# Optimization experiments

Hardware: AMD Instinct MI355X
Metric: run time of the kernel (lower is better)

## Reference

```python
import jax, jax.numpy as jnp
import numpy as np

R, D, H, NLAYERS = 128, 64, 64, 3
B, N = 64, 1024
INIT_W = 0.1


def setup_inputs() -> dict:
    key = jax.random.key(0)
    ks = jax.random.split(key, 10)
    x = jax.random.normal(ks[0], (B, D, N), dtype=jnp.float32)
    L = jax.random.randint(ks[1], (B, 1, N), 0, 2, dtype=jnp.int32)
    wq0 = INIT_W * jax.random.normal(ks[2], (R, D), dtype=jnp.float32)
    wqr = INIT_W * jax.random.normal(ks[3], (NLAYERS - 1, R, R), dtype=jnp.float32)
    wk0 = INIT_W * jax.random.normal(ks[4], (R, D), dtype=jnp.float32)
    wkr = INIT_W * jax.random.normal(ks[5], (NLAYERS - 1, R, R), dtype=jnp.float32)
    wv0 = INIT_W * jax.random.normal(ks[6], (R, D), dtype=jnp.float32)
    wvr = INIT_W * jax.random.normal(ks[7], (NLAYERS - 1, R, R), dtype=jnp.float32)
    wor = INIT_W * jax.random.normal(ks[8], (NLAYERS - 1, R, R), dtype=jnp.float32)
    wo_last = INIT_W * jax.random.normal(ks[9], (H, R), dtype=jnp.float32)
    return {"x": x, "L": L, "wq0": wq0, "wqr": wqr, "wk0": wk0, "wkr": wkr,
            "wv0": wv0, "wvr": wvr, "wor": wor, "wo_last": wo_last}


def reference(x, L, wq0, wqr, wk0, wkr, wv0, wvr, wor, wo_last):
    # x: [B, d, N]; L: [B, 1, N] neighbor mask (first row used)
    Lrow = L[:, 0, :].astype(jnp.float32)                      # [B, N]
    num_neighbors = jnp.sum((Lrow >= 1).astype(jnp.float32), axis=1)[:, None, None] + 1.0  # [B,1,1]
    scale = jnp.sqrt(num_neighbors)
    mask = Lrow[:, None, :]                                    # [B, 1, N], broadcast over r

    inp = x
    for layer in range(NLAYERS):
        Wq = wq0 if layer == 0 else wqr[layer - 1]
        Wk = wk0 if layer == 0 else wkr[layer - 1]
        Wv = wv0 if layer == 0 else wvr[layer - 1]
        # sigmoid-gated projections: [B, r, N]
        Q = jax.nn.sigmoid(jnp.einsum('rd,bdn->brn', Wq, inp))
        K = jax.nn.sigmoid(jnp.einsum('rd,bdn->brn', Wk, inp))
        V = jax.nn.sigmoid(jnp.einsum('rd,bdn->brn', Wv, inp))
        # degree-scaled softmax attention over agents: scores [B, N, N]
        A = jax.nn.softmax(jnp.einsum('brn,brm->bnm', Q, K) / scale, axis=-1)
        # o[b,r,n] = sum_m A[b,n,m] * V[b,r,m]  -> [B, r, N]
        o = jnp.einsum('bnm,brm->brn', A, V)
        Wo = wor[layer] if layer < NLAYERS - 1 else wo_last
        inp = jax.nn.silu(jnp.einsum('or,brn->bon', Wo, o))
        if layer != NLAYERS - 1:  # remask_bias=True
            inp = mask * inp
    return inp  # [B, h, N]
```

## Files before the change

kernel.cpp:

```cpp
#include <hip/hip_runtime.h>


typedef __bf16 bf16;
typedef bf16 bf16x2 __attribute__((ext_vector_type(2)));
typedef bf16 bf16x4 __attribute__((ext_vector_type(4)));
typedef bf16 bf16x8 __attribute__((ext_vector_type(8)));
typedef float f32x4 __attribute__((ext_vector_type(4)));
typedef float f32x16 __attribute__((ext_vector_type(16)));
typedef unsigned int u32;
typedef u32 u32x4 __attribute__((ext_vector_type(4)));

#define MFMA32(a, b, c) __builtin_amdgcn_mfma_f32_32x32x16_bf16(a, b, c, 0, 0, 0)
#define ZERO16 {0,0,0,0,0,0,0,0,0,0,0,0,0,0,0,0}
#define LOG2E 1.44269504f

__device__ __forceinline__ float fast_exp2(float x) {
  return __builtin_amdgcn_exp2f(x);
}
__device__ __forceinline__ float fast_sigmoid(float x) {
  return __builtin_amdgcn_rcpf(1.0f + fast_exp2(-LOG2E * x));
}
__device__ __forceinline__ u32 cvt_pk_bf16(float lo, float hi) {
  u32 r;
  asm("v_cvt_pk_bf16_f32 %0, %1, %2" : "=v"(r) : "v"(lo), "v"(hi));
  return r;
}
__device__ __forceinline__ void pl32_swap(u32& a, u32& b) {
  asm("v_permlane32_swap_b32 %0, %1" : "+v"(a), "+v"(b));
}
__device__ __forceinline__ void build_frags(const f32x16 v, bf16x8& f0, bf16x8& f1) {
  u32 t0 = cvt_pk_bf16(v[0], v[1]);
  u32 t1 = cvt_pk_bf16(v[2], v[3]);
  u32 t2 = cvt_pk_bf16(v[4], v[5]);
  u32 t3 = cvt_pk_bf16(v[6], v[7]);
  pl32_swap(t0, t2);
  pl32_swap(t1, t3);
  u32x4 a = {t0, t1, t2, t3};
  f0 = __builtin_bit_cast(bf16x8, a);
  u32 s0 = cvt_pk_bf16(v[8], v[9]);
  u32 s1 = cvt_pk_bf16(v[10], v[11]);
  u32 s2 = cvt_pk_bf16(v[12], v[13]);
  u32 s3 = cvt_pk_bf16(v[14], v[15]);
  pl32_swap(s0, s2);
  pl32_swap(s1, s3);
  u32x4 c = {s0, s1, s2, s3};
  f1 = __builtin_bit_cast(bf16x8, c);
}

__global__ __launch_bounds__(256) void prep_kernel(
    const int* __restrict__ L,
    const float* __restrict__ wq0, const float* __restrict__ wqr,
    const float* __restrict__ wk0, const float* __restrict__ wkr,
    const float* __restrict__ wv0, const float* __restrict__ wvr,
    const float* __restrict__ wor, const float* __restrict__ wo_last,
    float* __restrict__ scale_inv, float* __restrict__ biasv,
    bf16* __restrict__ wbf) {
  __shared__ int red[256];
  const int blk = blockIdx.x;
  const int tid = threadIdx.x;
  if (blk < 64) {
    int cnt = 0;
    for (int n = tid; n < 1024; n += 256) cnt += (L[blk * 1024 + n] >= 1) ? 1 : 0;
    red[tid] = cnt;
    __syncthreads();
    for (int s = 128; s > 0; s >>= 1) {
      if (tid < s) red[tid] += red[tid + s];
      __syncthreads();
    }
    if (tid == 0) {
      float iv = rsqrtf((float)red[0] + 1.0f);
      scale_inv[blk] = iv;
      biasv[blk] = fmaxf(0.0f, 128.0f * iv * LOG2E - 80.0f);
    }
  } else {
    for (int i = (blk - 64) * 256 + tid; i < 163840; i += 64 * 256) {
      float v;
      if      (i <   8192) v = wq0[i];
      else if (i <  40960) v = wqr[i - 8192];
      else if (i <  49152) v = wk0[i - 40960];
      else if (i <  81920) v = wkr[i - 49152];
      else if (i <  90112) v = wv0[i - 81920];
      else if (i < 122880) v = wvr[i - 90112];
      else if (i < 155648) v = wor[i - 122880];
      else                 v = wo_last[i - 155648];
      wbf[i] = (bf16)v;
    }
  }
}

__global__ __launch_bounds__(256) void xk0_kernel(
    const float* __restrict__ x, const bf16* __restrict__ Wk,
    const bf16* __restrict__ Wv, bf16* __restrict__ xT,
    bf16* __restrict__ Kt, bf16* __restrict__ Vn) {
  __shared__ float tile[64][65];
  __shared__ __attribute__((aligned(16))) bf16 inp_lds[64 * 72];
  const int tid = threadIdx.x;
  const int lane = tid & 63, wv = tid >> 6;
  const int la = lane & 31, hi = lane >> 5;
  const int b = blockIdx.x >> 4;
  const int t0 = (blockIdx.x & 15) * 64;

  {
    const int nl = tid & 63, dbase = (tid >> 6) * 16;
#pragma unroll
    for (int i = 0; i < 16; i++) {
      int d = dbase + i;
      tile[d][nl] = x[(size_t)(b * 64 + d) * 1024 + t0 + nl];
    }
  }
  __syncthreads();
  {
    const int dl = (tid & 31) * 2, nb = (tid >> 5) * 8;
#pragma unroll
    for (int i = 0; i < 8; i++) {
      int n = nb + i;
      bf16x2 pr = {(bf16)tile[dl][n], (bf16)tile[dl + 1][n]};
      *(bf16x2*)(xT + (size_t)(b * 1024 + t0 + n) * 64 + dl) = pr;
      *(bf16x2*)&inp_lds[n * 72 + dl] = pr;
    }
  }
  __syncthreads();

  const int sub = wv & 1;
  if (wv < 2) {
#pragma unroll
    for (int rt2 = 0; rt2 < 2; rt2++) {
      const int rt = 2 * sub + rt2;
      bf16x8 wf[4];
#pragma unroll
      for (int ks = 0; ks < 4; ks++)
        wf[ks] = *(const bf16x8*)(Wk + (size_t)(la + 32 * rt) * 64 + hi * 8 + ks * 16);
#pragma unroll
      for (int tt = 0; tt < 2; tt++) {
        f32x16 acc = ZERO16;
#pragma unroll
        for (int ks = 0; ks < 4; ks++) {
          bf16x8 bfr = *(const bf16x8*)&inp_lds[(la + 32 * tt) * 72 + hi * 8 + ks * 16];
          acc = MFMA32(wf[ks], bfr, acc);
        }
#pragma unroll
        for (int g = 0; g < 4; g++) {
          bf16x4 pk;
#pragma unroll
          for (int i = 0; i < 4; i++) pk[i] = (bf16)fast_sigmoid(acc[4 * g + i]);
          *(bf16x4*)(Kt + (size_t)(b * 1024 + t0 + 32 * tt + la) * 128 +
                     32 * rt + 8 * g + 4 * hi) = pk;
        }
      }
    }
  } else {
#pragma unroll
    for (int rc2 = 0; rc2 < 2; rc2++) {
      const int rc = 2 * sub + rc2;
      bf16x8 wf[4];
#pragma unroll
      for (int ks = 0; ks < 4; ks++)
        wf[ks] = *(const bf16x8*)(Wv + (size_t)(la + 32 * rc) * 64 + hi * 8 + ks * 16);
#pragma unroll
      for (int tt = 0; tt < 2; tt++) {
        f32x16 acc = ZERO16;
#pragma unroll
        for (int ks = 0; ks < 4; ks++) {
          bf16x8 afr = *(const bf16x8*)&inp_lds[(la + 32 * tt) * 72 + hi * 8 + ks * 16];
          acc = MFMA32(afr, wf[ks], acc);
        }
#pragma unroll
        for (int g = 0; g < 4; g++) {
          bf16x4 pk;
#pragma unroll
          for (int i = 0; i < 4; i++) pk[i] = (bf16)fast_sigmoid(acc[4 * g + i]);
          *(bf16x4*)(Vn + (size_t)(b * 128 + la + 32 * rc) * 1024 +
                     t0 + 32 * tt + 8 * g + 4 * hi) = pk;
        }
      }
    }
  }
}

template <int DIN>
__global__ __launch_bounds__(256) void kv_kernel(
    const bf16* __restrict__ inpT, const bf16* __restrict__ Wk,
    const bf16* __restrict__ Wv, bf16* __restrict__ Kt,
    bf16* __restrict__ Vn) {
  constexpr int SIN = DIN + 8;
  constexpr int KS = DIN / 16;
  constexpr int CPR = DIN / 8;
  __shared__ __attribute__((aligned(16))) bf16 inp_lds[64 * SIN];
  const int tid = threadIdx.x;
  const int lane = tid & 63, wv = tid >> 6;
  const int la = lane & 31, hi = lane >> 5;
  const int b = blockIdx.x >> 4;
  const int t0 = (blockIdx.x & 15) * 64;

  for (int i = tid; i < 64 * CPR; i += 256) {
    int row = i / CPR, c = i % CPR;
    *(bf16x8*)&inp_lds[row * SIN + c * 8] =
        *(const bf16x8*)(inpT + (size_t)(b * 1024 + t0 + row) * DIN + c * 8);
  }
  __syncthreads();

  const int sub = wv & 1;
  if (wv < 2) {
#pragma unroll
    for (int rt2 = 0; rt2 < 2; rt2++) {
      const int rt = 2 * sub + rt2;
      bf16x8 wf[KS];
#pragma unroll
      for (int ks = 0; ks < KS; ks++)
        wf[ks] = *(const bf16x8*)(Wk + (size_t)(la + 32 * rt) * DIN + hi * 8 + ks * 16);
#pragma unroll
      for (int tt = 0; tt < 2; tt++) {
        f32x16 acc = ZERO16;
#pragma unroll
        for (int ks = 0; ks < KS; ks++) {
          bf16x8 bfr = *(const bf16x8*)&inp_lds[(la + 32 * tt) * SIN + hi * 8 + ks * 16];
          acc = MFMA32(wf[ks], bfr, acc);
        }
#pragma unroll
        for (int g = 0; g < 4; g++) {
          bf16x4 pk;
#pragma unroll
          for (int i = 0; i < 4; i++) pk[i] = (bf16)fast_sigmoid(acc[4 * g + i]);
          *(bf16x4*)(Kt + (size_t)(b * 1024 + t0 + 32 * tt + la) * 128 +
                     32 * rt + 8 * g + 4 * hi) = pk;
        }
      }
    }
  } else {
#pragma unroll
    for (int rc2 = 0; rc2 < 2; rc2++) {
      const int rc = 2 * sub + rc2;
      bf16x8 wf[KS];
#pragma unroll
      for (int ks = 0; ks < KS; ks++)
        wf[ks] = *(const bf16x8*)(Wv + (size_t)(la + 32 * rc) * DIN + hi * 8 + ks * 16);
#pragma unroll
      for (int tt = 0; tt < 2; tt++) {
        f32x16 acc = ZERO16;
#pragma unroll
        for (int ks = 0; ks < KS; ks++) {
          bf16x8 afr = *(const bf16x8*)&inp_lds[(la + 32 * tt) * SIN + hi * 8 + ks * 16];
          acc = MFMA32(afr, wf[ks], acc);
        }
#pragma unroll
        for (int g = 0; g < 4; g++) {
          bf16x4 pk;
#pragma unroll
          for (int i = 0; i < 4; i++) pk[i] = (bf16)fast_sigmoid(acc[4 * g + i]);
          *(bf16x4*)(Vn + (size_t)(b * 128 + 32 * rc + la) * 1024 +
                     t0 + 32 * tt + 8 * g + 4 * hi) = pk;
        }
      }
    }
  }
}

template <int DIN>
__global__ __launch_bounds__(256, 2) void flash_kernel(
    const bf16* __restrict__ inpT, const bf16* __restrict__ Wq,
    const bf16* __restrict__ Kt, const bf16* __restrict__ Vn,
    const float* __restrict__ scale_inv, const float* __restrict__ biasv,
    const int* __restrict__ L, const bf16* __restrict__ Wo,
    void* __restrict__ outp, int last,
    const bf16* __restrict__ Wkn, const bf16* __restrict__ Wvn,
    bf16* __restrict__ Ktn, bf16* __restrict__ Vnn, int kvgen) {
  __shared__ __attribute__((aligned(16))) char smem[71680];

  const int tid = threadIdx.x;
  const int lane = tid & 63, wv = tid >> 6;
  const int la = lane & 31, hi = lane >> 5;
  const int xcd = blockIdx.x & 7;
  const int kk = blockIdx.x >> 3;
  const int b = xcd * 8 + (kk & 7);
  const int q0 = (kk >> 3) * 128;

  const float inv2 = scale_inv[b] * LOG2E;
  const float bb = biasv[b];

  const int krow = tid >> 4, kc = (tid & 15) * 8;
  const int vrow = tid >> 3, vc = (tid & 7) * 8;
  const bf16* kbase = Kt + (size_t)b * 1024 * 128;
  const bf16* vbase = Vn + (size_t)b * 128 * 1024;

  bf16x8 kr[4], vr[4];
#pragma unroll
  for (int p = 0; p < 4; p++) {
    kr[p] = *(const bf16x8*)(kbase + (size_t)(krow + 16 * p) * 128 + kc);
    vr[p] = *(const bf16x8*)(vbase + (size_t)(vrow + 32 * p) * 1024 + vc);
  }

  bf16x8 qB[8];
  {
    constexpr int SIN = DIN + 8;
    constexpr int KSD = DIN / 16;
    constexpr int CPR = DIN / 8;
    bf16* inp_s = (bf16*)smem;
    for (int i = tid; i < 128 * CPR; i += 256) {
      int row = i / CPR, c = i % CPR;
      *(bf16x8*)&inp_s[row * SIN + c * 8] =
          *(const bf16x8*)(inpT + (size_t)(b * 1024 + q0 + row) * DIN + c * 8);
    }
    __syncthreads();
    bf16x8 bfr[KSD];
#pragma unroll
    for (int ks = 0; ks < KSD; ks++)
      bfr[ks] = *(const bf16x8*)&inp_s[(32 * wv + la) * SIN + hi * 8 + ks * 16];
#pragma unroll
    for (int rt = 0; rt < 4; rt++) {
      f32x16 acc = ZERO16;
#pragma unroll
      for (int ks = 0; ks < KSD; ks++) {
        bf16x8 wf = *(const bf16x8*)(Wq + (size_t)(32 * rt + la) * DIN +
                                     hi * 8 + ks * 16);
        acc = MFMA32(wf, bfr[ks], acc);
      }
      f32x16 qv;
#pragma unroll
      for (int j = 0; j < 16; j++) qv[j] = fast_sigmoid(acc[j]) * inv2;
      build_frags(qv, qB[2 * rt], qB[2 * rt + 1]);
    }
    __syncthreads();
  }

  {
    bf16* K0 = (bf16*)smem;
    bf16* V0 = (bf16*)(smem + 34816);
#pragma unroll
    for (int p = 0; p < 4; p++) *(bf16x8*)&K0[(krow + 16 * p) * 136 + kc] = kr[p];
#pragma unroll
    for (int p = 0; p < 4; p++) *(bf16x8*)&V0[(vrow + 32 * p) * 72 + vc] = vr[p];
#pragma unroll
    for (int p = 0; p < 4; p++) {
      kr[p] = *(const bf16x8*)(kbase + (size_t)(64 + krow + 16 * p) * 128 + kc);
      vr[p] = *(const bf16x8*)(vbase + (size_t)(vrow + 32 * p) * 1024 + 64 + vc);
    }
    __syncthreads();
  }

  f32x16 acc_o[4] = {ZERO16, ZERO16, ZERO16, ZERO16};
  float rs = 0.f;

  for (int it = 0; it < 16; it++) {
    const int cur = it & 1;
    const bf16* Kc = (const bf16*)(smem + cur * 17408);
    const bf16* Vc = (const bf16*)(smem + 34816 + cur * 18432);
    if (it < 15) {
      bf16* Kn = (bf16*)(smem + (1 - cur) * 17408);
      bf16* Vx = (bf16*)(smem + 34816 + (1 - cur) * 18432);
#pragma unroll
      for (int p = 0; p < 4; p++)
        *(bf16x8*)&Kn[(krow + 16 * p) * 136 + kc] = kr[p];
#pragma unroll
      for (int p = 0; p < 4; p++)
        *(bf16x8*)&Vx[(vrow + 32 * p) * 72 + vc] = vr[p];
    }
    if (it < 14) {
      const int m2 = (it + 2) * 64;
#pragma unroll
      for (int p = 0; p < 4; p++) {
        kr[p] = *(const bf16x8*)(kbase + (size_t)(m2 + krow + 16 * p) * 128 + kc);
        vr[p] = *(const bf16x8*)(vbase + (size_t)(vrow + 32 * p) * 1024 + m2 + vc);
      }
    }

    bf16x8 pa[4];
#pragma unroll
    for (int kt = 0; kt < 2; kt++) {
      f32x16 sa = ZERO16;
#pragma unroll
      for (int ks = 0; ks < 8; ks++) {
        bf16x8 kf = *(const bf16x8*)&Kc[(32 * kt + la) * 136 + hi * 8 + ks * 16];
        sa = MFMA32(kf, qB[ks], sa);
      }
      f32x16 pv;
#pragma unroll
      for (int j = 0; j < 16; j++) {
        float p = fast_exp2(sa[j] - bb);
        rs += p;
        pv[j] = p;
      }
      build_frags(pv, pa[2 * kt], pa[2 * kt + 1]);
    }

#pragma unroll
    for (int rt = 0; rt < 4; rt++) {
#pragma unroll
      for (int k2 = 0; k2 < 4; k2++) {
        bf16x8 vB = *(const bf16x8*)&Vc[(32 * rt + la) * 72 + hi * 8 + k2 * 16];
        acc_o[rt] = MFMA32(pa[k2], vB, acc_o[rt]);
      }
    }
    __syncthreads();
  }

  rs += __shfl_xor(rs, 32, 64);
  float* rsp = (float*)(smem + 34816);
  if (lane < 32) rsp[32 * wv + la] = rs;
  bf16* O_lds = (bf16*)smem;
#pragma unroll
  for (int g = 0; g < 4; g++) {
    const int qb = 8 * g + 4 * hi;
    f32x4 r4 = *(f32x4*)&rsp[32 * wv + qb];
    f32x4 is;
#pragma unroll
    for (int i = 0; i < 4; i++) is[i] = 1.0f / r4[i];
#pragma unroll
    for (int rt = 0; rt < 4; rt++) {
#pragma unroll
      for (int i = 0; i < 4; i++) {
        O_lds[(size_t)(32 * wv + qb + i) * 136 + 32 * rt + la] =
            (bf16)(acc_o[rt][4 * g + i] * is[i]);
      }
    }
  }
  __syncthreads();

  if (!last) {
    bf16* out_b = (bf16*)outp;
    bf16* O2 = (bf16*)(smem + 36864);
    const int* Lg = L + b * 1024 + q0;
    bf16x8 wB[8];
#pragma unroll
    for (int ks = 0; ks < 8; ks++)
      wB[ks] = *(const bf16x8*)(Wo + (size_t)(la + 32 * wv) * 128 + hi * 8 + ks * 16);
#pragma unroll
    for (int nt = 0; nt < 4; nt++) {
      f32x16 acc = ZERO16;
#pragma unroll
      for (int ks = 0; ks < 8; ks++) {
        bf16x8 oA = *(const bf16x8*)&O_lds[(size_t)(la + 32 * nt) * 136 +
                                           hi * 8 + ks * 16];
        acc = MFMA32(oA, wB[ks], acc);
      }
#pragma unroll
      for (int g = 0; g < 4; g++) {
#pragma unroll
        for (int i = 0; i < 4; i++) {
          int n = 32 * nt + 8 * g + 4 * hi + i;
          float xv = acc[4 * g + i];
          float y = xv * fast_sigmoid(xv) * (float)Lg[n];
          out_b[(size_t)(b * 1024 + q0 + n) * 128 + 32 * wv + la] = (bf16)y;
          if (kvgen) O2[(size_t)n * 136 + 32 * wv + la] = (bf16)y;
        }
      }
    }
    if (kvgen) {
      __syncthreads();
      const bf16* O2c = (const bf16*)(smem + 36864);
      const int sub = wv & 1;
      const bf16* W2 = (wv < 2) ? Wkn : Wvn;
#pragma unroll
      for (int rt2 = 0; rt2 < 2; rt2++) {
        const int rt = 2 * sub + rt2;
        bf16x8 wf[8];
#pragma unroll
        for (int ks = 0; ks < 8; ks++)
          wf[ks] = *(const bf16x8*)(W2 + (size_t)(la + 32 * rt) * 128 +
                                    hi * 8 + ks * 16);
#pragma unroll
        for (int tt = 0; tt < 4; tt++) {
          f32x16 acc = ZERO16;
          if (wv < 2) {
#pragma unroll
            for (int ks = 0; ks < 8; ks++) {
              bf16x8 bB = *(const bf16x8*)&O2c[(size_t)(32 * tt + la) * 136 +
                                               hi * 8 + ks * 16];
              acc = MFMA32(wf[ks], bB, acc);
            }
#pragma unroll
            for (int g = 0; g < 4; g++) {
              bf16x4 pk;
#pragma unroll
              for (int i = 0; i < 4; i++) pk[i] = (bf16)fast_sigmoid(acc[4 * g + i]);
              *(bf16x4*)(Ktn + (size_t)(b * 1024 + q0 + 32 * tt + la) * 128 +
                         32 * rt + 8 * g + 4 * hi) = pk;
            }
          } else {
#pragma unroll
            for (int ks = 0; ks < 8; ks++) {
              bf16x8 aA = *(const bf16x8*)&O2c[(size_t)(32 * tt + la) * 136 +
                                               hi * 8 + ks * 16];
              acc = MFMA32(aA, wf[ks], acc);
            }
#pragma unroll
            for (int g = 0; g < 4; g++) {
              bf16x4 pk;
#pragma unroll
              for (int i = 0; i < 4; i++) pk[i] = (bf16)fast_sigmoid(acc[4 * g + i]);
              *(bf16x4*)(Vnn + (size_t)(b * 128 + 32 * rt + la) * 1024 +
                         q0 + 32 * tt + 8 * g + 4 * hi) = pk;
            }
          }
        }
      }
    }
  } else {
    const int hs = wv & 1, nq = wv >> 1;
    float* outf = (float*)outp;
    bf16x8 wA[8];
#pragma unroll
    for (int ks = 0; ks < 8; ks++)
      wA[ks] = *(const bf16x8*)(Wo + (size_t)(la + 32 * hs) * 128 + hi * 8 + ks * 16);
#pragma unroll
    for (int t = 0; t < 2; t++) {
      const int ns4 = nq + 2 * t;
      f32x16 acc = ZERO16;
#pragma unroll
      for (int ks = 0; ks < 8; ks++) {
        bf16x8 oB = *(const bf16x8*)&O_lds[(size_t)(32 * ns4 + la) * 136 +
                                           hi * 8 + ks * 16];
        acc = MFMA32(wA[ks], oB, acc);
      }
#pragma unroll
      for (int g = 0; g < 4; g++) {
#pragma unroll
        for (int i = 0; i < 4; i++) {
          int h = 32 * hs + 8 * g + 4 * hi + i;
          float xv = acc[4 * g + i];
          outf[(size_t)(b * 64 + h) * 1024 + q0 + 32 * ns4 + la] =
              xv * fast_sigmoid(xv);
        }
      }
    }
  }
}

__global__ __launch_bounds__(256) void xpose_kernel(const float* __restrict__ x,
                                                    bf16* __restrict__ xT) {
  __shared__ float tile[64][65];
  const int blk = blockIdx.x;
  const int b = blk >> 4;
  const int n0 = (blk & 15) * 64;
  const int tid = threadIdx.x;
  {
    const int nl = tid & 63, dbase = (tid >> 6) * 16;
#pragma unroll
    for (int i = 0; i < 16; i++) {
      int d = dbase + i;
      tile[d][nl] = x[(size_t)(b * 64 + d) * 1024 + n0 + nl];
    }
  }
  __syncthreads();
  {
    const int dl = (tid & 31) * 2, nb = (tid >> 5) * 8;
#pragma unroll
    for (int i = 0; i < 8; i++) {
      int n = nb + i;
      bf16x2 pr = {(bf16)tile[dl][n], (bf16)tile[dl + 1][n]};
      *(bf16x2*)(xT + (size_t)(b * 1024 + n0 + n) * 64 + dl) = pr;
    }
  }
}

extern "C" void kernel_launch(void* const* d_in, const int* in_sizes, int n_in,
                              void* d_out, int out_size, void* d_ws, size_t ws_size,
                              hipStream_t stream) {
  const float* x = (const float*)d_in[0];
  const int* L = (const int*)d_in[1];
  const float* wq0 = (const float*)d_in[2];
  const float* wqr = (const float*)d_in[3];
  const float* wk0 = (const float*)d_in[4];
  const float* wkr = (const float*)d_in[5];
  const float* wv0 = (const float*)d_in[6];
  const float* wvr = (const float*)d_in[7];
  const float* wor = (const float*)d_in[8];
  const float* wo_last = (const float*)d_in[9];

  char* ws = (char*)d_ws;
  float* scale_inv = (float*)(ws + 0);
  float* biasv = (float*)(ws + 1024);
  bf16* wbf = (bf16*)(ws + 4096);
  bf16* xT = (bf16*)(ws + 335872);
  bf16* inpT = (bf16*)(ws + 8724480);
  bf16* KtA = (bf16*)(ws + 25501696);
  bf16* VnA = (bf16*)(ws + 42278912);
  bf16* KtB = (bf16*)(ws + 59056128);
  bf16* VnB = (bf16*)(ws + 75833344);

  prep_kernel<<<128, 256, 0, stream>>>(L, wq0, wqr, wk0, wkr, wv0, wvr, wor,
                                       wo_last, scale_inv, biasv, wbf);

  if (ws_size >= 92610560) {
    xk0_kernel<<<1024, 256, 0, stream>>>(x, wbf + 40960, wbf + 81920, xT, KtA, VnA);
    flash_kernel<64><<<512, 256, 0, stream>>>(
        xT, wbf + 0, KtA, VnA, scale_inv, biasv, L, wbf + 122880, (void*)inpT, 0,
        wbf + 49152, wbf + 90112, KtB, VnB, 1);
    flash_kernel<128><<<512, 256, 0, stream>>>(
        inpT, wbf + 8192, KtB, VnB, scale_inv, biasv, L, wbf + 139264,
        (void*)inpT, 0, wbf + 65536, wbf + 106496, KtA, VnA, 1);
    flash_kernel<128><<<512, 256, 0, stream>>>(
        inpT, wbf + 24576, KtA, VnA, scale_inv, biasv, L, wbf + 155648, d_out, 1,
        nullptr, nullptr, nullptr, nullptr, 0);
  } else if (ws_size >= 59056128) {
    xpose_kernel<<<1024, 256, 0, stream>>>(x, xT);
    for (int l = 0; l < 3; l++) {
      const bf16* Wq = (l == 0) ? wbf + 0 : wbf + 8192 + (size_t)(l - 1) * 16384;
      const bf16* Wk = (l == 0) ? wbf + 40960 : wbf + 49152 + (size_t)(l - 1) * 16384;
      const bf16* Wv = (l == 0) ? wbf + 81920 : wbf + 90112 + (size_t)(l - 1) * 16384;
      const bf16* Wo = (l < 2) ? wbf + 122880 + (size_t)l * 16384 : wbf + 155648;
      void* outp = (l < 2) ? (void*)inpT : (void*)d_out;
      if (l == 0) {
        kv_kernel<64><<<1024, 256, 0, stream>>>(xT, Wk, Wv, KtA, VnA);
        flash_kernel<64><<<512, 256, 0, stream>>>(xT, Wq, KtA, VnA, scale_inv,
                                                  biasv, L, Wo, outp, 0,
                                                  nullptr, nullptr, nullptr,
                                                  nullptr, 0);
      } else {
        kv_kernel<128><<<1024, 256, 0, stream>>>(inpT, Wk, Wv, KtA, VnA);
        flash_kernel<128><<<512, 256, 0, stream>>>(inpT, Wq, KtA, VnA, scale_inv,
                                                   biasv, L, Wo, outp,
                                                   (l == 2) ? 1 : 0, nullptr,
                                                   nullptr, nullptr, nullptr, 0);
      }
    }
  }
}
```

Measured before the change: 273.6 us.

## Split flash kernel into 64-query tiles with intra-block KV split and reduction

Each block now handles 64 queries instead of 128, and the grid doubles to 1024 blocks. Inside a block, the four waves split into two query tiles and two key halves, and the key-half partial outputs and row sums are combined through LDS at the end. The K/V double buffer is replaced by a single buffer with two barriers per step, halving shared memory so launch bounds can request three blocks per CU. The aim is more parallelism and occupancy, at the cost of extra synchronisation, a cross-wave reduction, and twice the K/V global reads per query.

```diff
diff --git a/kernel.cpp b/kernel.cpp
--- a/kernel.cpp
+++ b/kernel.cpp
@@ -45,6 +45,12 @@
   pl32_swap(s1, s3);
   u32x4 c = {s0, s1, s2, s3};
   f1 = __builtin_bit_cast(bf16x8, c);
+}
+__device__ __forceinline__ float treesum16(const f32x16 v) {
+  float a0 = v[0] + v[1], a1 = v[2] + v[3], a2 = v[4] + v[5], a3 = v[6] + v[7];
+  float a4 = v[8] + v[9], a5 = v[10] + v[11], a6 = v[12] + v[13], a7 = v[14] + v[15];
+  float b0 = a0 + a1, b1 = a2 + a3, b2 = a4 + a5, b3 = a6 + a7;
+  return (b0 + b1) + (b2 + b3);
 }
 
 __global__ __launch_bounds__(256) void prep_kernel(
@@ -256,7 +262,7 @@
 }
 
 template <int DIN>
-__global__ __launch_bounds__(256, 2) void flash_kernel(
+__global__ __launch_bounds__(256, 3) void flash_kernel(
     const bf16* __restrict__ inpT, const bf16* __restrict__ Wq,
     const bf16* __restrict__ Kt, const bf16* __restrict__ Vn,
     const float* __restrict__ scale_inv, const float* __restrict__ biasv,
@@ -264,15 +270,16 @@
     void* __restrict__ outp, int last,
     const bf16* __restrict__ Wkn, const bf16* __restrict__ Wvn,
     bf16* __restrict__ Ktn, bf16* __restrict__ Vnn, int kvgen) {
-  __shared__ __attribute__((aligned(16))) char smem[71680];
+  __shared__ __attribute__((aligned(16))) char smem[35840];
 
   const int tid = threadIdx.x;
   const int lane = tid & 63, wv = tid >> 6;
   const int la = lane & 31, hi = lane >> 5;
+  const int qt = wv & 1, kg = wv >> 1;
   const int xcd = blockIdx.x & 7;
   const int kk = blockIdx.x >> 3;
   const int b = xcd * 8 + (kk & 7);
-  const int q0 = (kk >> 3) * 128;
+  const int q0 = (kk >> 3) * 64;
 
   const float inv2 = scale_inv[b] * LOG2E;
   const float bb = biasv[b];
@@ -295,7 +302,7 @@
     constexpr int KSD = DIN / 16;
     constexpr int CPR = DIN / 8;
     bf16* inp_s = (bf16*)smem;
-    for (int i = tid; i < 128 * CPR; i += 256) {
+    for (int i = tid; i < 64 * CPR; i += 256) {
       int row = i / CPR, c = i % CPR;
       *(bf16x8*)&inp_s[row * SIN + c * 8] =
           *(const bf16x8*)(inpT + (size_t)(b * 1024 + q0 + row) * DIN + c * 8);
@@ -304,7 +311,7 @@
     bf16x8 bfr[KSD];
 #pragma unroll
     for (int ks = 0; ks < KSD; ks++)
-      bfr[ks] = *(const bf16x8*)&inp_s[(32 * wv + la) * SIN + hi * 8 + ks * 16];
+      bfr[ks] = *(const bf16x8*)&inp_s[(32 * qt + la) * SIN + hi * 8 + ks * 16];
 #pragma unroll
     for (int rt = 0; rt < 4; rt++) {
       f32x16 acc = ZERO16;
@@ -319,97 +326,107 @@
       for (int j = 0; j < 16; j++) qv[j] = fast_sigmoid(acc[j]) * inv2;
       build_frags(qv, qB[2 * rt], qB[2 * rt + 1]);
     }
-    __syncthreads();
-  }
-
-  {
-    bf16* K0 = (bf16*)smem;
-    bf16* V0 = (bf16*)(smem + 34816);
-#pragma unroll
-    for (int p = 0; p < 4; p++) *(bf16x8*)&K0[(krow + 16 * p) * 136 + kc] = kr[p];
-#pragma unroll
-    for (int p = 0; p < 4; p++) *(bf16x8*)&V0[(vrow + 32 * p) * 72 + vc] = vr[p];
-#pragma unroll
-    for (int p = 0; p < 4; p++) {
-      kr[p] = *(const bf16x8*)(kbase + (size_t)(64 + krow + 16 * p) * 128 + kc);
-      vr[p] = *(const bf16x8*)(vbase + (size_t)(vrow + 32 * p) * 1024 + 64 + vc);
-    }
-    __syncthreads();
-  }
-
+  }
+
+  bf16* K_lds = (bf16*)smem;
+  bf16* V_lds = (bf16*)(smem + 17408);
   f32x16 acc_o[4] = {ZERO16, ZERO16, ZERO16, ZERO16};
   float rs = 0.f;
 
   for (int it = 0; it < 16; it++) {
-    const int cur = it & 1;
-    const bf16* Kc = (const bf16*)(smem + cur * 17408);
-    const bf16* Vc = (const bf16*)(smem + 34816 + cur * 18432);
+    __syncthreads();
+#pragma unroll
+    for (int p = 0; p < 4; p++)
+      *(bf16x8*)&K_lds[(krow + 16 * p) * 136 + kc] = kr[p];
+#pragma unroll
+    for (int p = 0; p < 4; p++)
+      *(bf16x8*)&V_lds[(vrow + 32 * p) * 72 + vc] = vr[p];
+    __syncthreads();
+
+    f32x16 sa = ZERO16;
+#pragma unroll
+    for (int ks = 0; ks < 8; ks++) {
+      bf16x8 kf = *(const bf16x8*)&K_lds[(32 * kg + la) * 136 + hi * 8 + ks * 16];
+      sa = MFMA32(kf, qB[ks], sa);
+    }
+
+    f32x16 pv;
+#pragma unroll
+    for (int j = 0; j < 16; j++) pv[j] = fast_exp2(sa[j] - bb);
+    rs += treesum16(pv);
+    bf16x8 pa[2];
+    build_frags(pv, pa[0], pa[1]);
+
     if (it < 15) {
-      bf16* Kn = (bf16*)(smem + (1 - cur) * 17408);
-      bf16* Vx = (bf16*)(smem + 34816 + (1 - cur) * 18432);
-#pragma unroll
-      for (int p = 0; p < 4; p++)
-        *(bf16x8*)&Kn[(krow + 16 * p) * 136 + kc] = kr[p];
-#pragma unroll
-      for (int p = 0; p < 4; p++)
-        *(bf16x8*)&Vx[(vrow + 32 * p) * 72 + vc] = vr[p];
-    }
-    if (it < 14) {
-      const int m2 = (it + 2) * 64;
+      const int m1 = (it + 1) * 64;
 #pragma unroll
       for (int p = 0; p < 4; p++) {
-        kr[p] = *(const bf16x8*)(kbase + (size_t)(m2 + krow + 16 * p) * 128 + kc);
-        vr[p] = *(const bf16x8*)(vbase + (size_t)(vrow + 32 * p) * 1024 + m2 + vc);
-      }
-    }
-
-    bf16x8 pa[4];
-#pragma unroll
-    for (int kt = 0; kt < 2; kt++) {
-      f32x16 sa = ZERO16;
-#pragma unroll
-      for (int ks = 0; ks < 8; ks++) {
-        bf16x8 kf = *(const bf16x8*)&Kc[(32 * kt + la) * 136 + hi * 8 + ks * 16];
-        sa = MFMA32(kf, qB[ks], sa);
-      }
-      f32x16 pv;
-#pragma unroll
-      for (int j = 0; j < 16; j++) {
-        float p = fast_exp2(sa[j] - bb);
-        rs += p;
-        pv[j] = p;
-      }
-      build_frags(pv, pa[2 * kt], pa[2 * kt + 1]);
+        kr[p] = *(const bf16x8*)(kbase + (size_t)(m1 + krow + 16 * p) * 128 + kc);
+        vr[p] = *(const bf16x8*)(vbase + (size_t)(vrow + 32 * p) * 1024 + m1 + vc);
+      }
     }
 
 #pragma unroll
     for (int rt = 0; rt < 4; rt++) {
 #pragma unroll
-      for (int k2 = 0; k2 < 4; k2++) {
-        bf16x8 vB = *(const bf16x8*)&Vc[(32 * rt + la) * 72 + hi * 8 + k2 * 16];
+      for (int k2 = 0; k2 < 2; k2++) {
+        bf16x8 vB = *(const bf16x8*)&V_lds[(32 * rt + la) * 72 +
+                                           32 * kg + 16 * k2 + 8 * hi];
         acc_o[rt] = MFMA32(pa[k2], vB, acc_o[rt]);
       }
     }
-    __syncthreads();
   }
 
   rs += __shfl_xor(rs, 32, 64);
-  float* rsp = (float*)(smem + 34816);
-  if (lane < 32) rsp[32 * wv + la] = rs;
+  float* hand = (float*)smem;
+  float* rsc = (float*)(smem + 34816);
+  __syncthreads();
+  if (kg) {
+    float* dst = hand + qt * 4352 + lane * 68;
+#pragma unroll
+    for (int rt = 0; rt < 4; rt++) {
+#pragma unroll
+      for (int q4 = 0; q4 < 4; q4++) {
+        f32x4 t = {acc_o[rt][4 * q4], acc_o[rt][4 * q4 + 1],
+                   acc_o[rt][4 * q4 + 2], acc_o[rt][4 * q4 + 3]};
+        *(f32x4*)(dst + 16 * rt + 4 * q4) = t;
+      }
+    }
+    if (lane < 32) rsc[qt * 32 + la] = rs;
+  }
+  __syncthreads();
+  if (kg == 0) {
+    const float* src = hand + qt * 4352 + lane * 68;
+#pragma unroll
+    for (int rt = 0; rt < 4; rt++) {
+#pragma unroll
+      for (int q4 = 0; q4 < 4; q4++) {
+        f32x4 t = *(const f32x4*)(src + 16 * rt + 4 * q4);
+#pragma unroll
+        for (int i = 0; i < 4; i++) acc_o[rt][4 * q4 + i] += t[i];
+      }
+    }
+    rs += rsc[qt * 32 + la];
+    if (lane < 32) rsc[qt * 32 + la] = rs;
+  }
+  __syncthreads();
+
   bf16* O_lds = (bf16*)smem;
-#pragma unroll
-  for (int g = 0; g < 4; g++) {
-    const int qb = 8 * g + 4 * hi;
-    f32x4 r4 = *(f32x4*)&rsp[32 * wv + qb];
-    f32x4 is;
-#pragma unroll
-    for (int i = 0; i < 4; i++) is[i] = 1.0f / r4[i];
-#pragma unroll
-    for (int rt = 0; rt < 4; rt++) {
-#pragma unroll
-      for (int i = 0; i < 4; i++) {
-        O_lds[(size_t)(32 * wv + qb + i) * 136 + 32 * rt + la] =
-            (bf16)(acc_o[rt][4 * g + i] * is[i]);
+  if (kg == 0) {
+#pragma unroll
+    for (int g = 0; g < 4; g++) {
+      const int qb = 8 * g + 4 * hi;
+      f32x4 r4 = *(f32x4*)&rsc[32 * qt + qb];
+      f32x4 is;
+#pragma unroll
+      for (int i = 0; i < 4; i++) is[i] = 1.0f / r4[i];
+#pragma unroll
+      for (int rt = 0; rt < 4; rt++) {
+#pragma unroll
+        for (int i = 0; i < 4; i++) {
+          O_lds[(size_t)(32 * qt + qb + i) * 136 + 32 * rt + la] =
+              (bf16)(acc_o[rt][4 * g + i] * is[i]);
+        }
       }
     }
   }
@@ -417,18 +434,18 @@
 
   if (!last) {
     bf16* out_b = (bf16*)outp;
-    bf16* O2 = (bf16*)(smem + 36864);
+    bf16* O2 = (bf16*)(smem + 17408);
     const int* Lg = L + b * 1024 + q0;
     bf16x8 wB[8];
 #pragma unroll
     for (int ks = 0; ks < 8; ks++)
       wB[ks] = *(const bf16x8*)(Wo + (size_t)(la + 32 * wv) * 128 + hi * 8 + ks * 16);
 #pragma unroll
-    for (int nt = 0; nt < 4; nt++) {
+    for (int tt = 0; tt < 2; tt++) {
       f32x16 acc = ZERO16;
 #pragma unroll
       for (int ks = 0; ks < 8; ks++) {
-        bf16x8 oA = *(const bf16x8*)&O_lds[(size_t)(la + 32 * nt) * 136 +
+        bf16x8 oA = *(const bf16x8*)&O_lds[(size_t)(la + 32 * tt) * 136 +
                                            hi * 8 + ks * 16];
         acc = MFMA32(oA, wB[ks], acc);
       }
@@ -436,7 +453,7 @@
       for (int g = 0; g < 4; g++) {
 #pragma unroll
         for (int i = 0; i < 4; i++) {
-          int n = 32 * nt + 8 * g + 4 * hi + i;
+          int n = 32 * tt + 8 * g + 4 * hi + i;
           float xv = acc[4 * g + i];
           float y = xv * fast_sigmoid(xv) * (float)Lg[n];
           out_b[(size_t)(b * 1024 + q0 + n) * 128 + 32 * wv + la] = (bf16)y;
@@ -446,80 +463,80 @@
     }
     if (kvgen) {
       __syncthreads();
-      const bf16* O2c = (const bf16*)(smem + 36864);
-      const int sub = wv & 1;
-      const bf16* W2 = (wv < 2) ? Wkn : Wvn;
-#pragma unroll
-      for (int rt2 = 0; rt2 < 2; rt2++) {
-        const int rt = 2 * sub + rt2;
+      const bf16* O2c = (const bf16*)(smem + 17408);
+      {
         bf16x8 wf[8];
 #pragma unroll
         for (int ks = 0; ks < 8; ks++)
-          wf[ks] = *(const bf16x8*)(W2 + (size_t)(la + 32 * rt) * 128 +
+          wf[ks] = *(const bf16x8*)(Wkn + (size_t)(la + 32 * wv) * 128 +
                                     hi * 8 + ks * 16);
 #pragma unroll
-        for (int tt = 0; tt < 4; tt++) {
+        for (int tt = 0; tt < 2; tt++) {
           f32x16 acc = ZERO16;
-          if (wv < 2) {
-#pragma unroll
-            for (int ks = 0; ks < 8; ks++) {
-              bf16x8 bB = *(const bf16x8*)&O2c[(size_t)(32 * tt + la) * 136 +
-                                               hi * 8 + ks * 16];
-              acc = MFMA32(wf[ks], bB, acc);
-            }
-#pragma unroll
-            for (int g = 0; g < 4; g++) {
-              bf16x4 pk;
-#pragma unroll
-              for (int i = 0; i < 4; i++) pk[i] = (bf16)fast_sigmoid(acc[4 * g + i]);
-              *(bf16x4*)(Ktn + (size_t)(b * 1024 + q0 + 32 * tt + la) * 128 +
-                         32 * rt + 8 * g + 4 * hi) = pk;
-            }
-          } else {
-#pragma unroll
-            for (int ks = 0; ks < 8; ks++) {
-              bf16x8 aA = *(const bf16x8*)&O2c[(size_t)(32 * tt + la) * 136 +
-                                               hi * 8 + ks * 16];
-              acc = MFMA32(aA, wf[ks], acc);
-            }
-#pragma unroll
-            for (int g = 0; g < 4; g++) {
-              bf16x4 pk;
-#pragma unroll
-              for (int i = 0; i < 4; i++) pk[i] = (bf16)fast_sigmoid(acc[4 * g + i]);
-              *(bf16x4*)(Vnn + (size_t)(b * 128 + 32 * rt + la) * 1024 +
-                         q0 + 32 * tt + 8 * g + 4 * hi) = pk;
-            }
+#pragma unroll
+          for (int ks = 0; ks < 8; ks++) {
+            bf16x8 bB = *(const bf16x8*)&O2c[(size_t)(32 * tt + la) * 136 +
+                                             hi * 8 + ks * 16];
+            acc = MFMA32(wf[ks], bB, acc);
           }
+#pragma unroll
+          for (int g = 0; g < 4; g++) {
+            bf16x4 pk;
+#pragma unroll
+            for (int i = 0; i < 4; i++) pk[i] = (bf16)fast_sigmoid(acc[4 * g + i]);
+            *(bf16x4*)(Ktn + (size_t)(b * 1024 + q0 + 32 * tt + la) * 128 +
+                       32 * wv + 8 * g + 4 * hi) = pk;
+          }
+        }
+      }
+      {
+        bf16x8 wf[8];
+#pragma unroll
+        for (int ks = 0; ks < 8; ks++)
+          wf[ks] = *(const bf16x8*)(Wvn + (size_t)(la + 32 * wv) * 128 +
+                                    hi * 8 + ks * 16);
+#pragma unroll
+        for (int tt = 0; tt < 2; tt++) {
+          f32x16 acc = ZERO16;
+#pragma unroll
+          for (int ks = 0; ks < 8; ks++) {
+            bf16x8 aA = *(const bf16x8*)&O2c[(size_t)(32 * tt + la) * 136 +
+                                             hi * 8 + ks * 16];
+            acc = MFMA32(aA, wf[ks], acc);
+          }
+#pragma unroll
+          for (int g = 0; g < 4; g++) {
+            bf16x4 pk;
+#pragma unroll
+            for (int i = 0; i < 4; i++) pk[i] = (bf16)fast_sigmoid(acc[4 * g + i]);
+            *(bf16x4*)(Vnn + (size_t)(b * 128 + 32 * wv + la) * 1024 +
+                       q0 + 32 * tt + 8 * g + 4 * hi) = pk;
+          }
         }
       }
     }
   } else {
-    const int hs = wv & 1, nq = wv >> 1;
+    const int hs = wv & 1, nt = wv >> 1;
     float* outf = (float*)outp;
     bf16x8 wA[8];
 #pragma unroll
     for (int ks = 0; ks < 8; ks++)
       wA[ks] = *(const bf16x8*)(Wo + (size_t)(la + 32 * hs) * 128 + hi * 8 + ks * 16);
-#pragma unroll
-    for (int t = 0; t < 2; t++) {
-      const int ns4 = nq + 2 * t;
-      f32x16 acc = ZERO16;
-#pragma unroll
-      for (int ks = 0; ks < 8; ks++) {
-        bf16x8 oB = *(const bf16x8*)&O_lds[(size_t)(32 * ns4 + la) * 136 +
-                                           hi * 8 + ks * 16];
-        acc = MFMA32(wA[ks], oB, acc);
-      }
-#pragma unroll
-      for (int g = 0; g < 4; g++) {
-#pragma unroll
-        for (int i = 0; i < 4; i++) {
-          int h = 32 * hs + 8 * g + 4 * hi + i;
-          float xv = acc[4 * g + i];
-          outf[(size_t)(b * 64 + h) * 1024 + q0 + 32 * ns4 + la] =
-              xv * fast_sigmoid(xv);
-        }
+    f32x16 acc = ZERO16;
+#pragma unroll
+    for (int ks = 0; ks < 8; ks++) {
+      bf16x8 oB = *(const bf16x8*)&O_lds[(size_t)(32 * nt + la) * 136 +
+                                         hi * 8 + ks * 16];
+      acc = MFMA32(wA[ks], oB, acc);
+    }
+#pragma unroll
+    for (int g = 0; g < 4; g++) {
+#pragma unroll
+      for (int i = 0; i < 4; i++) {
+        int h = 32 * hs + 8 * g + 4 * hi + i;
+        float xv = acc[4 * g + i];
+        outf[(size_t)(b * 64 + h) * 1024 + q0 + 32 * nt + la] =
+            xv * fast_sigmoid(xv);
       }
     }
   }
@@ -582,13 +599,13 @@
 
   if (ws_size >= 92610560) {
     xk0_kernel<<<1024, 256, 0, stream>>>(x, wbf + 40960, wbf + 81920, xT, KtA, VnA);
-    flash_kernel<64><<<512, 256, 0, stream>>>(
+    flash_kernel<64><<<1024, 256, 0, stream>>>(
         xT, wbf + 0, KtA, VnA, scale_inv, biasv, L, wbf + 122880, (void*)inpT, 0,
         wbf + 49152, wbf + 90112, KtB, VnB, 1);
-    flash_kernel<128><<<512, 256, 0, stream>>>(
+    flash_kernel<128><<<1024, 256, 0, stream>>>(
         inpT, wbf + 8192, KtB, VnB, scale_inv, biasv, L, wbf + 139264,
         (void*)inpT, 0, wbf + 65536, wbf + 106496, KtA, VnA, 1);
-    flash_kernel<128><<<512, 256, 0, stream>>>(
+    flash_kernel<128><<<1024, 256, 0, stream>>>(
         inpT, wbf + 24576, KtA, VnA, scale_inv, biasv, L, wbf + 155648, d_out, 1,
         nullptr, nullptr, nullptr, nullptr, 0);
   } else if (ws_size >= 59056128) {
@@ -601,17 +618,17 @@
       void* outp = (l < 2) ? (void*)inpT : (void*)d_out;
       if (l == 0) {
         kv_kernel<64><<<1024, 256, 0, stream>>>(xT, Wk, Wv, KtA, VnA);
-        flash_kernel<64><<<512, 256, 0, stream>>>(xT, Wq, KtA, VnA, scale_inv,
-                                                  biasv, L, Wo, outp, 0,
-                                                  nullptr, nullptr, nullptr,
-                                                  nullptr, 0);
+        flash_kernel<64><<<1024, 256, 0, stream>>>(xT, Wq, KtA, VnA, scale_inv,
+                                                   biasv, L, Wo, outp, 0,
+                                                   nullptr, nullptr, nullptr,
+                                                   nullptr, 0);
       } else {
         kv_kernel<128><<<1024, 256, 0, stream>>>(inpT, Wk, Wv, KtA, VnA);
-        flash_kernel<128><<<512, 256, 0, stream>>>(inpT, Wq, KtA, VnA, scale_inv,
-                                                   biasv, L, Wo, outp,
-                                                   (l == 2) ? 1 : 0, nullptr,
-                                                   nullptr, nullptr, nullptr, 0);
-      }
-    }
-  }
-}
+        flash_kernel<128><<<1024, 256, 0, stream>>>(inpT, Wq, KtA, VnA, scale_inv,
+                                                    biasv, L, Wo, outp,
+                                                    (l == 2) ? 1 : 0, nullptr,
+                                                    nullptr, nullptr, nullptr, 0);
+      }
+    }
+  }
+}
```

After: 318.7 us. 16.5% more time.
